# Performance work log

Measured on AMD Instinct MI355X. Metric: run time of the kernel, lower is better.

The kernel has to match this reference:

```python
import jax, jax.numpy as jnp
import numpy as np

EPS = 1e-5
ALPHA = 0.2  # leaky relu negative slope


def instance_norm(x):
    # x: [b, n, c]; torch InstanceNorm1d normalizes each (b, c) over the n dim (no affine)
    mean = jnp.mean(x, axis=1, keepdims=True)
    var = jnp.var(x, axis=1, keepdims=True)
    return (x - mean) * jax.lax.rsqrt(var + EPS)


def gat_layer(x, w, a_src, a_dst, bias):
    # x: [b, n, f_in], w: [h, f_in, f_out], a_src/a_dst: [h, f_out, 1], bias: [f_out]
    h_prime = jnp.einsum('bnf,hfo->bhno', x, w)              # [b, h, n, f_out]
    attn_src = jnp.einsum('bhno,hoi->bhni', h_prime, a_src)[..., 0]  # [b, h, n]
    attn_dst = jnp.einsum('bhno,hoi->bhni', h_prime, a_dst)[..., 0]  # [b, h, n]
    # outer-sum additive attention: attn[b,h,i,j] = src[b,h,i] + dst[b,h,j]
    attn = attn_src[:, :, :, None] + attn_dst[:, :, None, :]
    attn = jnp.where(attn >= 0, attn, ALPHA * attn)          # leaky relu
    attn = jax.nn.softmax(attn, axis=-1)
    out = jnp.einsum('bhnm,bhmo->bhno', attn, h_prime) + bias
    return out


def setup_inputs() -> dict:
    key = jax.random.key(0)
    ks = jax.random.split(key, 9)
    b, n = 16, 1024
    f0, f1, f2 = 32, 16, 32   # n_units
    h0, h1 = 4, 1             # n_heads

    def xavier(k, shape, gain=1.414):
        fan_in, fan_out = shape[-2], shape[-1]
        a = gain * np.sqrt(6.0 / (fan_in + fan_out))
        return jax.random.uniform(k, shape, jnp.float32, -a, a)

    return {
        'x': jax.random.normal(ks[0], (b, n, f0), jnp.float32),
        'w1': xavier(ks[1], (h0, f0, f1)),
        'a_src1': xavier(ks[2], (h0, f1, 1)),
        'a_dst1': xavier(ks[3], (h0, f1, 1)),
        'b1': jnp.zeros((f1,), jnp.float32),
        'w2': xavier(ks[4], (h1, f1 * h0, f2)),
        'a_src2': xavier(ks[5], (h1, f2, 1)),
        'a_dst2': xavier(ks[6], (h1, f2, 1)),
        'b2': jnp.zeros((f2,), jnp.float32),
    }


def reference(x, w1, a_src1, a_dst1, b1, w2, a_src2, a_dst2, b2):
    b, n = x.shape[:2]
    # layer 0
    x = instance_norm(x)
    out = gat_layer(x, w1, a_src1, a_dst1, b1)               # [b, h0, n, f1]
    x = jnp.transpose(out, (0, 2, 1, 3)).reshape(b, n, -1)   # [b, n, h0*f1]
    x = jax.nn.elu(x)
    # layer 1 (last): squeeze head dim
    x = instance_norm(x)
    out = gat_layer(x, w2, a_src2, a_dst2, b2)               # [b, 1, n, f2]
    return out[:, 0]                                          # [b, n, f2]
```

## Files before the change

### kernel.cpp

```cpp
#include <hip/hip_runtime.h>


namespace {
constexpr int Nn  = 1024;
constexpr int F0  = 32;
constexpr int F1n = 16;
constexpr int FH  = 64;
constexpr int F2n = 32;
constexpr float LOG2E = 1.4426950408889634f;
constexpr float EPS   = 1e-5f;
constexpr float ALPHA = 0.2f;
}

typedef __attribute__((ext_vector_type(8))) _Float16 half8;
typedef __attribute__((ext_vector_type(4))) float f32x4;

__global__ __launch_bounds__(256) void k_proj1(
    const float* __restrict__ x, const float* __restrict__ w1,
    const float* __restrict__ asrc, const float* __restrict__ adst,
    short* __restrict__ hpT_hi, short* __restrict__ hpT_lo,
    float* __restrict__ src, float* __restrict__ dst,
    float* __restrict__ statsAcc)
{
  const int b    = blockIdx.x >> 4;
  const int tile = blockIdx.x & 15;
  const int t    = threadIdx.x;
  const int r    = t & 63, h = t >> 6;

  __shared__ float  s_sum[8][33];
  __shared__ float  s_ssq[8][33];
  __shared__ float  s_mean[32], s_rstd[32];
  __shared__ float4 s_wt4[4 * F1n * (F0 / 4)];
  __shared__ float  s_as[64], s_ad[64];

  if (tile == 0 && t < 128) statsAcc[b * 128 + t] = 0.f;

  float* s_wt = reinterpret_cast<float*>(s_wt4);
  for (int idx = t; idx < 4 * F1n * F0; idx += 256) {
    const int f = idx & 31, ho = idx >> 5;
    s_wt[idx] = w1[((ho >> 4) * F0 + f) * F1n + (ho & 15)];
  }
  if (t < 64) { s_as[t] = asrc[t]; s_ad[t] = adst[t]; }

  const float* xb = x + (size_t)b * Nn * F0;
  {
    const int c = t & 31, seg = t >> 5;
    float sum = 0.f, ssq = 0.f;
#pragma unroll 8
    for (int nn = seg; nn < Nn; nn += 8) {
      float v = xb[nn * F0 + c];
      sum += v; ssq += v * v;
    }
    s_sum[seg][c] = sum; s_ssq[seg][c] = ssq;
  }
  __syncthreads();
  if (t < 32) {
    float s = 0.f, q = 0.f;
#pragma unroll
    for (int k = 0; k < 8; k++) { s += s_sum[k][t]; q += s_ssq[k][t]; }
    const float mean = s * (1.f / Nn);
    const float var  = fmaf(-mean, mean, q * (1.f / Nn));
    s_mean[t] = mean;
    s_rstd[t] = rsqrtf(var + EPS);
  }
  __syncthreads();

  const int n  = tile * 64 + r;
  const int bh = b * 4 + h;
  float4 xr[F0 / 4];
  const float4* xrow = reinterpret_cast<const float4*>(xb + (size_t)n * F0);
#pragma unroll
  for (int k = 0; k < F0 / 4; k++) {
    float4 v = xrow[k];
    v.x = (v.x - s_mean[k * 4 + 0]) * s_rstd[k * 4 + 0];
    v.y = (v.y - s_mean[k * 4 + 1]) * s_rstd[k * 4 + 1];
    v.z = (v.z - s_mean[k * 4 + 2]) * s_rstd[k * 4 + 2];
    v.w = (v.w - s_mean[k * 4 + 3]) * s_rstd[k * 4 + 3];
    xr[k] = v;
  }

  float sdot = 0.f, ddot = 0.f;
#pragma unroll 1
  for (int o = 0; o < F1n; o++) {
    float acc = 0.f;
#pragma unroll
    for (int k = 0; k < F0 / 4; k++) {
      const float4 wv = s_wt4[(h * F1n + o) * (F0 / 4) + k];
      const float4 xv = xr[k];
      acc = fmaf(xv.x, wv.x, acc); acc = fmaf(xv.y, wv.y, acc);
      acc = fmaf(xv.z, wv.z, acc); acc = fmaf(xv.w, wv.w, acc);
    }
    sdot = fmaf(acc, s_as[h * F1n + o], sdot);
    ddot = fmaf(acc, s_ad[h * F1n + o], ddot);
    const _Float16 hh = (_Float16)acc;
    const _Float16 hl = (_Float16)(acc - (float)hh);
    const size_t idx = ((size_t)bh * F1n + o) * Nn + n;
    hpT_hi[idx] = __builtin_bit_cast(short, hh);
    hpT_lo[idx] = __builtin_bit_cast(short, hl);
  }
  src[bh * Nn + n] = sdot;
  dst[bh * Nn + n] = ddot;
}

__global__ __launch_bounds__(256) void k_attn1(
    const short* __restrict__ hpT_hi, const short* __restrict__ hpT_lo,
    const float* __restrict__ src, const float* __restrict__ dst,
    const float* __restrict__ bias, float* __restrict__ x1,
    float* __restrict__ statsAcc)
{
  const int bh   = blockIdx.x >> 4;
  const int tile = blockIdx.x & 15;
  const int t    = threadIdx.x;
  const int w    = t >> 6;
  const int l    = t & 63;
  const int col  = l & 15;
  const int ks   = l >> 4;

  __shared__ float s_dst[Nn];
  __shared__ float s_red[4];
  __shared__ float s_ps[4][16];

  const float* dp = dst + bh * Nn;
  float lm = -1e30f;
  for (int j = t; j < Nn; j += 256) { float v = dp[j]; s_dst[j] = v; lm = fmaxf(lm, v); }
#pragma unroll
  for (int mask = 32; mask >= 1; mask >>= 1) lm = fmaxf(lm, __shfl_xor(lm, mask));
  if (l == 0) s_red[w] = lm;
  __syncthreads();
  const float dmax = fmaxf(fmaxf(s_red[0], s_red[1]), fmaxf(s_red[2], s_red[3]));

  const int i0 = tile * 64 + w * 16;
  const float si = src[bh * Nn + i0 + col];
  const float t0v = si + dmax;
  const float em  = fmaxf(t0v, ALPHA * t0v) * LOG2E;

  auto pexp = [&](float dv) {
    const float tt = si + dv;
    const float u  = fmaxf(tt, ALPHA * tt);
    return exp2f(fmaf(u, LOG2E, -em));
  };

  const half8* bph = reinterpret_cast<const half8*>(hpT_hi + (size_t)bh * F1n * Nn);
  const half8* bpl = reinterpret_cast<const half8*>(hpT_lo + (size_t)bh * F1n * Nn);
  f32x4 acc = {0.f, 0.f, 0.f, 0.f};
  float psum = 0.f;

#pragma unroll 2
  for (int jb = 0; jb < 32; ++jb) {
    const int jo = (jb << 5) | (ks << 3);
    const float4 dA = *reinterpret_cast<const float4*>(&s_dst[jo]);
    const float4 dB = *reinterpret_cast<const float4*>(&s_dst[jo + 4]);
    half8 af;
    const _Float16 q0 = (_Float16)pexp(dA.x); af[0] = q0;
    const _Float16 q1 = (_Float16)pexp(dA.y); af[1] = q1;
    const _Float16 q2 = (_Float16)pexp(dA.z); af[2] = q2;
    const _Float16 q3 = (_Float16)pexp(dA.w); af[3] = q3;
    const _Float16 q4 = (_Float16)pexp(dB.x); af[4] = q4;
    const _Float16 q5 = (_Float16)pexp(dB.y); af[5] = q5;
    const _Float16 q6 = (_Float16)pexp(dB.z); af[6] = q6;
    const _Float16 q7 = (_Float16)pexp(dB.w); af[7] = q7;
    psum += (((float)q0 + (float)q1) + ((float)q2 + (float)q3)) +
            (((float)q4 + (float)q5) + ((float)q6 + (float)q7));

    const half8 bh8 = bph[col * 128 + (jb << 2) + ks];
    const half8 bl8 = bpl[col * 128 + (jb << 2) + ks];
    acc = __builtin_amdgcn_mfma_f32_16x16x32_f16(af, bh8, acc, 0, 0, 0);
    acc = __builtin_amdgcn_mfma_f32_16x16x32_f16(af, bl8, acc, 0, 0, 0);
  }

  psum += __shfl_xor(psum, 16);
  psum += __shfl_xor(psum, 32);
  if (l < 16) s_ps[w][col] = psum;
  __syncthreads();

  const int b = bh >> 2, h = bh & 3;
  const float bc = bias[col];
  float sv = 0.f, sq = 0.f;
#pragma unroll
  for (int r = 0; r < 4; ++r) {
    const int row = ks * 4 + r;
    const float inv = 1.f / s_ps[w][row];
    float v = fmaf(acc[r], inv, bc);
    v = v > 0.f ? v : exp2f(v * LOG2E) - 1.f;
    x1[((size_t)(b * Nn + i0 + row)) * FH + h * F1n + col] = v;
    sv += v; sq += v * v;
  }
  sv += __shfl_xor(sv, 16); sq += __shfl_xor(sq, 16);
  sv += __shfl_xor(sv, 32); sq += __shfl_xor(sq, 32);
  if (l < 16) {
    const int ch = h * F1n + col;
    atomicAdd(&statsAcc[b * 128 + ch], sv);
    atomicAdd(&statsAcc[b * 128 + 64 + ch], sq);
  }
}

__global__ __launch_bounds__(256) void k_proj2(
    const float* __restrict__ x1, const float* __restrict__ statsAcc,
    const float* __restrict__ w2,
    const float* __restrict__ asrc, const float* __restrict__ adst,
    short* __restrict__ hpT_hi, short* __restrict__ hpT_lo,
    float* __restrict__ src, float* __restrict__ dst)
{
  const int b    = blockIdx.x >> 4;
  const int tile = blockIdx.x & 15;
  const int t    = threadIdx.x;
  const int r    = t & 63, og = t >> 6;

  __shared__ float  s_mean[64], s_rstd[64];
  __shared__ float4 s_wt4[F2n * (FH / 4)];
  __shared__ float  s_as[F2n], s_ad[F2n];
  __shared__ float  s_sd[4][64][2];

  float* s_wt = reinterpret_cast<float*>(s_wt4);
  for (int idx = t; idx < F2n * FH; idx += 256) {
    const int f = idx & 63, o = idx >> 6;
    s_wt[idx] = w2[f * F2n + o];
  }
  if (t < F2n) { s_as[t] = asrc[t]; s_ad[t] = adst[t]; }
  if (t < 64) {
    const float s = statsAcc[b * 128 + t];
    const float q = statsAcc[b * 128 + 64 + t];
    const float mean = s * (1.f / Nn);
    const float var  = fmaf(-mean, mean, q * (1.f / Nn));
    s_mean[t] = mean;
    s_rstd[t] = rsqrtf(var + EPS);
  }
  __syncthreads();

  const int n    = tile * 64 + r;
  const int base = b * Nn + n;
  float4 xr[FH / 4];
  const float4* xrow = reinterpret_cast<const float4*>(
      x1 + (size_t)b * Nn * FH + (size_t)n * FH);
#pragma unroll
  for (int k = 0; k < FH / 4; k++) {
    float4 v = xrow[k];
    v.x = (v.x - s_mean[k * 4 + 0]) * s_rstd[k * 4 + 0];
    v.y = (v.y - s_mean[k * 4 + 1]) * s_rstd[k * 4 + 1];
    v.z = (v.z - s_mean[k * 4 + 2]) * s_rstd[k * 4 + 2];
    v.w = (v.w - s_mean[k * 4 + 3]) * s_rstd[k * 4 + 3];
    xr[k] = v;
  }

  float sdot = 0.f, ddot = 0.f;
#pragma unroll 1
  for (int oo = 0; oo < 8; oo++) {
    const int o = og * 8 + oo;
    float acc = 0.f;
#pragma unroll
    for (int k = 0; k < FH / 4; k++) {
      const float4 wv = s_wt4[o * (FH / 4) + k];
      const float4 xv = xr[k];
      acc = fmaf(xv.x, wv.x, acc); acc = fmaf(xv.y, wv.y, acc);
      acc = fmaf(xv.z, wv.z, acc); acc = fmaf(xv.w, wv.w, acc);
    }
    sdot = fmaf(acc, s_as[o], sdot);
    ddot = fmaf(acc, s_ad[o], ddot);
    const _Float16 hh = (_Float16)acc;
    const _Float16 hl = (_Float16)(acc - (float)hh);
    const size_t idx = ((size_t)b * F2n + o) * Nn + n;
    hpT_hi[idx] = __builtin_bit_cast(short, hh);
    hpT_lo[idx] = __builtin_bit_cast(short, hl);
  }

  s_sd[og][r][0] = sdot; s_sd[og][r][1] = ddot;
  __syncthreads();
  if (og == 0) {
    float s = 0.f, d = 0.f;
#pragma unroll
    for (int g = 0; g < 4; g++) { s += s_sd[g][r][0]; d += s_sd[g][r][1]; }
    src[base] = s;
    dst[base] = d;
  }
}

__global__ __launch_bounds__(256) void k_attn2(
    const short* __restrict__ hpT_hi, const short* __restrict__ hpT_lo,
    const float* __restrict__ src, const float* __restrict__ dst,
    const float* __restrict__ bias, float* __restrict__ out)
{
  const int b    = blockIdx.x >> 6;
  const int tile = blockIdx.x & 63;
  const int t    = threadIdx.x;
  const int jq   = t >> 6;
  const int l    = t & 63;
  const int col  = l & 15;
  const int ks   = l >> 4;

  __shared__ float s_dst[Nn];
  __shared__ float s_red[4];
  __shared__ float s_comb[3][64][9];
  __shared__ float s_ps[16];

  const float* dp = dst + b * Nn;
  float lm = -1e30f;
  for (int j = t; j < Nn; j += 256) { float v = dp[j]; s_dst[j] = v; lm = fmaxf(lm, v); }
#pragma unroll
  for (int mask = 32; mask >= 1; mask >>= 1) lm = fmaxf(lm, __shfl_xor(lm, mask));
  if (l == 0) s_red[jq] = lm;
  __syncthreads();
  const float dmax = fmaxf(fmaxf(s_red[0], s_red[1]), fmaxf(s_red[2], s_red[3]));

  const int i0 = tile * 16;
  const float si = src[b * Nn + i0 + col];
  const float t0v = si + dmax;
  const float em  = fmaxf(t0v, ALPHA * t0v) * LOG2E;

  auto pexp = [&](float dv) {
    const float tt = si + dv;
    const float u  = fmaxf(tt, ALPHA * tt);
    return exp2f(fmaf(u, LOG2E, -em));
  };

  const half8* bph = reinterpret_cast<const half8*>(hpT_hi + (size_t)b * F2n * Nn);
  const half8* bpl = reinterpret_cast<const half8*>(hpT_lo + (size_t)b * F2n * Nn);
  f32x4 acc0 = {0.f, 0.f, 0.f, 0.f};
  f32x4 acc1 = {0.f, 0.f, 0.f, 0.f};
  float psum = 0.f;

#pragma unroll 2
  for (int kb = 0; kb < 8; ++kb) {
    const int jb = jq * 8 + kb;
    const int jo = (jb << 5) | (ks << 3);
    const float4 dA = *reinterpret_cast<const float4*>(&s_dst[jo]);
    const float4 dB = *reinterpret_cast<const float4*>(&s_dst[jo + 4]);
    half8 af;
    const _Float16 q0 = (_Float16)pexp(dA.x); af[0] = q0;
    const _Float16 q1 = (_Float16)pexp(dA.y); af[1] = q1;
    const _Float16 q2 = (_Float16)pexp(dA.z); af[2] = q2;
    const _Float16 q3 = (_Float16)pexp(dA.w); af[3] = q3;
    const _Float16 q4 = (_Float16)pexp(dB.x); af[4] = q4;
    const _Float16 q5 = (_Float16)pexp(dB.y); af[5] = q5;
    const _Float16 q6 = (_Float16)pexp(dB.z); af[6] = q6;
    const _Float16 q7 = (_Float16)pexp(dB.w); af[7] = q7;
    psum += (((float)q0 + (float)q1) + ((float)q2 + (float)q3)) +
            (((float)q4 + (float)q5) + ((float)q6 + (float)q7));

    const half8 bh0 = bph[col * 128 + (jb << 2) + ks];
    const half8 bl0 = bpl[col * 128 + (jb << 2) + ks];
    const half8 bh1 = bph[(col + 16) * 128 + (jb << 2) + ks];
    const half8 bl1 = bpl[(col + 16) * 128 + (jb << 2) + ks];
    acc0 = __builtin_amdgcn_mfma_f32_16x16x32_f16(af, bh0, acc0, 0, 0, 0);
    acc0 = __builtin_amdgcn_mfma_f32_16x16x32_f16(af, bl0, acc0, 0, 0, 0);
    acc1 = __builtin_amdgcn_mfma_f32_16x16x32_f16(af, bh1, acc1, 0, 0, 0);
    acc1 = __builtin_amdgcn_mfma_f32_16x16x32_f16(af, bl1, acc1, 0, 0, 0);
  }

  if (jq > 0) {
#pragma unroll
    for (int r = 0; r < 4; ++r) {
      s_comb[jq - 1][l][r]     = acc0[r];
      s_comb[jq - 1][l][r + 4] = acc1[r];
    }
    s_comb[jq - 1][l][8] = psum;
  }
  __syncthreads();

  if (jq == 0) {
#pragma unroll
    for (int g = 0; g < 3; ++g) {
#pragma unroll
      for (int r = 0; r < 4; ++r) {
        acc0[r] += s_comb[g][l][r];
        acc1[r] += s_comb[g][l][r + 4];
      }
      psum += s_comb[g][l][8];
    }
    psum += __shfl_xor(psum, 16);
    psum += __shfl_xor(psum, 32);
    if (l < 16) s_ps[col] = psum;

    const float bc0 = bias[col];
    const float bc1 = bias[col + 16];
#pragma unroll
    for (int r = 0; r < 4; ++r) {
      const int row = ks * 4 + r;
      const float inv = 1.f / s_ps[row];
      float* op = out + ((size_t)(b * Nn + i0 + row)) * F2n;
      op[col]      = fmaf(acc0[r], inv, bc0);
      op[col + 16] = fmaf(acc1[r], inv, bc1);
    }
  }
}

extern "C" void kernel_launch(void* const* d_in, const int* in_sizes, int n_in,
                              void* d_out, int out_size, void* d_ws, size_t ws_size,
                              hipStream_t stream) {
  (void)in_sizes; (void)n_in; (void)out_size; (void)ws_size;
  const float* x   = (const float*)d_in[0];
  const float* w1  = (const float*)d_in[1];
  const float* as1 = (const float*)d_in[2];
  const float* ad1 = (const float*)d_in[3];
  const float* b1  = (const float*)d_in[4];
  const float* w2  = (const float*)d_in[5];
  const float* as2 = (const float*)d_in[6];
  const float* ad2 = (const float*)d_in[7];
  const float* b2  = (const float*)d_in[8];
  float* out = (float*)d_out;

  float* ws = (float*)d_ws;
  short* hpT1_hi = (short*)ws;
  short* hpT1_lo = (short*)(ws + 524288);
  short* hpT2_hi = (short*)(ws + 1048576);
  short* hpT2_lo = (short*)(ws + 1048576 + 262144);
  float* x1      = ws + 1048576 + 524288;
  float* src1    = x1 + 1048576;
  float* dst1    = src1 + 65536;
  float* src2    = dst1 + 65536;
  float* dst2    = src2 + 16384;
  float* statsA  = dst2 + 16384;

  k_proj1<<<256, 256, 0, stream>>>(x, w1, as1, ad1, hpT1_hi, hpT1_lo, src1, dst1, statsA);
  k_attn1<<<1024, 256, 0, stream>>>(hpT1_hi, hpT1_lo, src1, dst1, b1, x1, statsA);
  k_proj2<<<256, 256, 0, stream>>>(x1, statsA, w2, as2, ad2, hpT2_hi, hpT2_lo, src2, dst2);
  k_attn2<<<1024, 256, 0, stream>>>(hpT2_hi, hpT2_lo, src2, dst2, b2, out);
}
```

Before: 142.3 us.

## Fuse four stage kernels into one persistent kernel with grid barriers

Merges the projection and attention stages of both layers into a single 1024-block kernel. The stages are separated by atomic-counter grid barriers, and a shared-memory union lets every stage reuse the same LDS. The aim is to remove three kernel launch boundaries and the drain/ramp gaps between them. In exchange it needs all 1024 blocks co-resident (4 per CU), which is checked via an occupancy query with a fallback to the original four launches. It also adds a memset and a host occupancy call on every launch, and spin-wait barriers that idle the 768 blocks doing nothing during the projection stages.

```diff
diff --git a/kernel.cpp b/kernel.cpp
--- a/kernel.cpp
+++ b/kernel.cpp
@@ -15,32 +15,44 @@
 typedef __attribute__((ext_vector_type(8))) _Float16 half8;
 typedef __attribute__((ext_vector_type(4))) float f32x4;
 
-__global__ __launch_bounds__(256) void k_proj1(
+union alignas(16) Smem {
+  struct { float sum[8][33], ssq[8][33], mean[32], rstd[32], wt[2048], as[64], ad[64]; } p1;
+  struct { float dst[Nn], red[4], ps[4][16]; } p2;
+  struct { float mean[64], rstd[64], wt[2048], as[32], ad[32], sd[4][64][2]; } p3;
+  struct { float dst[Nn], red[4], comb[3][64][9], ps[16]; } p4;
+};
+
+__device__ __forceinline__ void grid_barrier(unsigned* c, unsigned nblk) {
+  __syncthreads();
+  if (threadIdx.x == 0) {
+    __threadfence();
+    __hip_atomic_fetch_add(c, 1u, __ATOMIC_RELAXED, __HIP_MEMORY_SCOPE_AGENT);
+    while (__hip_atomic_load(c, __ATOMIC_RELAXED, __HIP_MEMORY_SCOPE_AGENT) < nblk)
+      __builtin_amdgcn_s_sleep(2);
+    __threadfence();
+  }
+  __syncthreads();
+}
+
+__device__ __forceinline__ void proj1_body(
+    int bid, int t, Smem& sm,
     const float* __restrict__ x, const float* __restrict__ w1,
     const float* __restrict__ asrc, const float* __restrict__ adst,
     short* __restrict__ hpT_hi, short* __restrict__ hpT_lo,
     float* __restrict__ src, float* __restrict__ dst,
     float* __restrict__ statsAcc)
 {
-  const int b    = blockIdx.x >> 4;
-  const int tile = blockIdx.x & 15;
-  const int t    = threadIdx.x;
+  const int b    = bid >> 4;
+  const int tile = bid & 15;
   const int r    = t & 63, h = t >> 6;
 
-  __shared__ float  s_sum[8][33];
-  __shared__ float  s_ssq[8][33];
-  __shared__ float  s_mean[32], s_rstd[32];
-  __shared__ float4 s_wt4[4 * F1n * (F0 / 4)];
-  __shared__ float  s_as[64], s_ad[64];
-
   if (tile == 0 && t < 128) statsAcc[b * 128 + t] = 0.f;
 
-  float* s_wt = reinterpret_cast<float*>(s_wt4);
   for (int idx = t; idx < 4 * F1n * F0; idx += 256) {
     const int f = idx & 31, ho = idx >> 5;
-    s_wt[idx] = w1[((ho >> 4) * F0 + f) * F1n + (ho & 15)];
-  }
-  if (t < 64) { s_as[t] = asrc[t]; s_ad[t] = adst[t]; }
+    sm.p1.wt[idx] = w1[((ho >> 4) * F0 + f) * F1n + (ho & 15)];
+  }
+  if (t < 64) { sm.p1.as[t] = asrc[t]; sm.p1.ad[t] = adst[t]; }
 
   const float* xb = x + (size_t)b * Nn * F0;
   {
@@ -51,17 +63,17 @@
       float v = xb[nn * F0 + c];
       sum += v; ssq += v * v;
     }
-    s_sum[seg][c] = sum; s_ssq[seg][c] = ssq;
+    sm.p1.sum[seg][c] = sum; sm.p1.ssq[seg][c] = ssq;
   }
   __syncthreads();
   if (t < 32) {
     float s = 0.f, q = 0.f;
 #pragma unroll
-    for (int k = 0; k < 8; k++) { s += s_sum[k][t]; q += s_ssq[k][t]; }
+    for (int k = 0; k < 8; k++) { s += sm.p1.sum[k][t]; q += sm.p1.ssq[k][t]; }
     const float mean = s * (1.f / Nn);
     const float var  = fmaf(-mean, mean, q * (1.f / Nn));
-    s_mean[t] = mean;
-    s_rstd[t] = rsqrtf(var + EPS);
+    sm.p1.mean[t] = mean;
+    sm.p1.rstd[t] = rsqrtf(var + EPS);
   }
   __syncthreads();
 
@@ -72,26 +84,27 @@
 #pragma unroll
   for (int k = 0; k < F0 / 4; k++) {
     float4 v = xrow[k];
-    v.x = (v.x - s_mean[k * 4 + 0]) * s_rstd[k * 4 + 0];
-    v.y = (v.y - s_mean[k * 4 + 1]) * s_rstd[k * 4 + 1];
-    v.z = (v.z - s_mean[k * 4 + 2]) * s_rstd[k * 4 + 2];
-    v.w = (v.w - s_mean[k * 4 + 3]) * s_rstd[k * 4 + 3];
+    v.x = (v.x - sm.p1.mean[k * 4 + 0]) * sm.p1.rstd[k * 4 + 0];
+    v.y = (v.y - sm.p1.mean[k * 4 + 1]) * sm.p1.rstd[k * 4 + 1];
+    v.z = (v.z - sm.p1.mean[k * 4 + 2]) * sm.p1.rstd[k * 4 + 2];
+    v.w = (v.w - sm.p1.mean[k * 4 + 3]) * sm.p1.rstd[k * 4 + 3];
     xr[k] = v;
   }
 
+  const float4* wt4 = reinterpret_cast<const float4*>(sm.p1.wt);
   float sdot = 0.f, ddot = 0.f;
 #pragma unroll 1
   for (int o = 0; o < F1n; o++) {
     float acc = 0.f;
 #pragma unroll
     for (int k = 0; k < F0 / 4; k++) {
-      const float4 wv = s_wt4[(h * F1n + o) * (F0 / 4) + k];
+      const float4 wv = wt4[(h * F1n + o) * (F0 / 4) + k];
       const float4 xv = xr[k];
       acc = fmaf(xv.x, wv.x, acc); acc = fmaf(xv.y, wv.y, acc);
       acc = fmaf(xv.z, wv.z, acc); acc = fmaf(xv.w, wv.w, acc);
     }
-    sdot = fmaf(acc, s_as[h * F1n + o], sdot);
-    ddot = fmaf(acc, s_ad[h * F1n + o], ddot);
+    sdot = fmaf(acc, sm.p1.as[h * F1n + o], sdot);
+    ddot = fmaf(acc, sm.p1.ad[h * F1n + o], ddot);
     const _Float16 hh = (_Float16)acc;
     const _Float16 hl = (_Float16)(acc - (float)hh);
     const size_t idx = ((size_t)bh * F1n + o) * Nn + n;
@@ -102,32 +115,29 @@
   dst[bh * Nn + n] = ddot;
 }
 
-__global__ __launch_bounds__(256) void k_attn1(
+__device__ __forceinline__ void attn1_body(
+    int bid, int t, Smem& sm,
     const short* __restrict__ hpT_hi, const short* __restrict__ hpT_lo,
     const float* __restrict__ src, const float* __restrict__ dst,
     const float* __restrict__ bias, float* __restrict__ x1,
     float* __restrict__ statsAcc)
 {
-  const int bh   = blockIdx.x >> 4;
-  const int tile = blockIdx.x & 15;
-  const int t    = threadIdx.x;
+  const int bh   = bid >> 4;
+  const int tile = bid & 15;
   const int w    = t >> 6;
   const int l    = t & 63;
   const int col  = l & 15;
   const int ks   = l >> 4;
 
-  __shared__ float s_dst[Nn];
-  __shared__ float s_red[4];
-  __shared__ float s_ps[4][16];
-
   const float* dp = dst + bh * Nn;
   float lm = -1e30f;
-  for (int j = t; j < Nn; j += 256) { float v = dp[j]; s_dst[j] = v; lm = fmaxf(lm, v); }
+  for (int j = t; j < Nn; j += 256) { float v = dp[j]; sm.p2.dst[j] = v; lm = fmaxf(lm, v); }
 #pragma unroll
   for (int mask = 32; mask >= 1; mask >>= 1) lm = fmaxf(lm, __shfl_xor(lm, mask));
-  if (l == 0) s_red[w] = lm;
-  __syncthreads();
-  const float dmax = fmaxf(fmaxf(s_red[0], s_red[1]), fmaxf(s_red[2], s_red[3]));
+  if (l == 0) sm.p2.red[w] = lm;
+  __syncthreads();
+  const float dmax = fmaxf(fmaxf(sm.p2.red[0], sm.p2.red[1]),
+                           fmaxf(sm.p2.red[2], sm.p2.red[3]));
 
   const int i0 = tile * 64 + w * 16;
   const float si = src[bh * Nn + i0 + col];
@@ -148,8 +158,8 @@
 #pragma unroll 2
   for (int jb = 0; jb < 32; ++jb) {
     const int jo = (jb << 5) | (ks << 3);
-    const float4 dA = *reinterpret_cast<const float4*>(&s_dst[jo]);
-    const float4 dB = *reinterpret_cast<const float4*>(&s_dst[jo + 4]);
+    const float4 dA = *reinterpret_cast<const float4*>(&sm.p2.dst[jo]);
+    const float4 dB = *reinterpret_cast<const float4*>(&sm.p2.dst[jo + 4]);
     half8 af;
     const _Float16 q0 = (_Float16)pexp(dA.x); af[0] = q0;
     const _Float16 q1 = (_Float16)pexp(dA.y); af[1] = q1;
@@ -170,7 +180,7 @@
 
   psum += __shfl_xor(psum, 16);
   psum += __shfl_xor(psum, 32);
-  if (l < 16) s_ps[w][col] = psum;
+  if (l < 16) sm.p2.ps[w][col] = psum;
   __syncthreads();
 
   const int b = bh >> 2, h = bh & 3;
@@ -179,7 +189,7 @@
 #pragma unroll
   for (int r = 0; r < 4; ++r) {
     const int row = ks * 4 + r;
-    const float inv = 1.f / s_ps[w][row];
+    const float inv = 1.f / sm.p2.ps[w][row];
     float v = fmaf(acc[r], inv, bc);
     v = v > 0.f ? v : exp2f(v * LOG2E) - 1.f;
     x1[((size_t)(b * Nn + i0 + row)) * FH + h * F1n + col] = v;
@@ -194,36 +204,30 @@
   }
 }
 
-__global__ __launch_bounds__(256) void k_proj2(
+__device__ __forceinline__ void proj2_body(
+    int bid, int t, Smem& sm,
     const float* __restrict__ x1, const float* __restrict__ statsAcc,
     const float* __restrict__ w2,
     const float* __restrict__ asrc, const float* __restrict__ adst,
     short* __restrict__ hpT_hi, short* __restrict__ hpT_lo,
     float* __restrict__ src, float* __restrict__ dst)
 {
-  const int b    = blockIdx.x >> 4;
-  const int tile = blockIdx.x & 15;
-  const int t    = threadIdx.x;
+  const int b    = bid >> 4;
+  const int tile = bid & 15;
   const int r    = t & 63, og = t >> 6;
 
-  __shared__ float  s_mean[64], s_rstd[64];
-  __shared__ float4 s_wt4[F2n * (FH / 4)];
-  __shared__ float  s_as[F2n], s_ad[F2n];
-  __shared__ float  s_sd[4][64][2];
-
-  float* s_wt = reinterpret_cast<float*>(s_wt4);
   for (int idx = t; idx < F2n * FH; idx += 256) {
     const int f = idx & 63, o = idx >> 6;
-    s_wt[idx] = w2[f * F2n + o];
-  }
-  if (t < F2n) { s_as[t] = asrc[t]; s_ad[t] = adst[t]; }
+    sm.p3.wt[idx] = w2[f * F2n + o];
+  }
+  if (t < F2n) { sm.p3.as[t] = asrc[t]; sm.p3.ad[t] = adst[t]; }
   if (t < 64) {
     const float s = statsAcc[b * 128 + t];
     const float q = statsAcc[b * 128 + 64 + t];
     const float mean = s * (1.f / Nn);
     const float var  = fmaf(-mean, mean, q * (1.f / Nn));
-    s_mean[t] = mean;
-    s_rstd[t] = rsqrtf(var + EPS);
+    sm.p3.mean[t] = mean;
+    sm.p3.rstd[t] = rsqrtf(var + EPS);
   }
   __syncthreads();
 
@@ -235,13 +239,14 @@
 #pragma unroll
   for (int k = 0; k < FH / 4; k++) {
     float4 v = xrow[k];
-    v.x = (v.x - s_mean[k * 4 + 0]) * s_rstd[k * 4 + 0];
-    v.y = (v.y - s_mean[k * 4 + 1]) * s_rstd[k * 4 + 1];
-    v.z = (v.z - s_mean[k * 4 + 2]) * s_rstd[k * 4 + 2];
-    v.w = (v.w - s_mean[k * 4 + 3]) * s_rstd[k * 4 + 3];
+    v.x = (v.x - sm.p3.mean[k * 4 + 0]) * sm.p3.rstd[k * 4 + 0];
+    v.y = (v.y - sm.p3.mean[k * 4 + 1]) * sm.p3.rstd[k * 4 + 1];
+    v.z = (v.z - sm.p3.mean[k * 4 + 2]) * sm.p3.rstd[k * 4 + 2];
+    v.w = (v.w - sm.p3.mean[k * 4 + 3]) * sm.p3.rstd[k * 4 + 3];
     xr[k] = v;
   }
 
+  const float4* wt4 = reinterpret_cast<const float4*>(sm.p3.wt);
   float sdot = 0.f, ddot = 0.f;
 #pragma unroll 1
   for (int oo = 0; oo < 8; oo++) {
@@ -249,13 +254,13 @@
     float acc = 0.f;
 #pragma unroll
     for (int k = 0; k < FH / 4; k++) {
-      const float4 wv = s_wt4[o * (FH / 4) + k];
+      const float4 wv = wt4[o * (FH / 4) + k];
       const float4 xv = xr[k];
       acc = fmaf(xv.x, wv.x, acc); acc = fmaf(xv.y, wv.y, acc);
       acc = fmaf(xv.z, wv.z, acc); acc = fmaf(xv.w, wv.w, acc);
     }
-    sdot = fmaf(acc, s_as[o], sdot);
-    ddot = fmaf(acc, s_ad[o], ddot);
+    sdot = fmaf(acc, sm.p3.as[o], sdot);
+    ddot = fmaf(acc, sm.p3.ad[o], ddot);
     const _Float16 hh = (_Float16)acc;
     const _Float16 hl = (_Float16)(acc - (float)hh);
     const size_t idx = ((size_t)b * F2n + o) * Nn + n;
@@ -263,43 +268,39 @@
     hpT_lo[idx] = __builtin_bit_cast(short, hl);
   }
 
-  s_sd[og][r][0] = sdot; s_sd[og][r][1] = ddot;
+  sm.p3.sd[og][r][0] = sdot; sm.p3.sd[og][r][1] = ddot;
   __syncthreads();
   if (og == 0) {
     float s = 0.f, d = 0.f;
 #pragma unroll
-    for (int g = 0; g < 4; g++) { s += s_sd[g][r][0]; d += s_sd[g][r][1]; }
+    for (int g = 0; g < 4; g++) { s += sm.p3.sd[g][r][0]; d += sm.p3.sd[g][r][1]; }
     src[base] = s;
     dst[base] = d;
   }
 }
 
-__global__ __launch_bounds__(256) void k_attn2(
+__device__ __forceinline__ void attn2_body(
+    int bid, int t, Smem& sm,
     const short* __restrict__ hpT_hi, const short* __restrict__ hpT_lo,
     const float* __restrict__ src, const float* __restrict__ dst,
     const float* __restrict__ bias, float* __restrict__ out)
 {
-  const int b    = blockIdx.x >> 6;
-  const int tile = blockIdx.x & 63;
-  const int t    = threadIdx.x;
+  const int b    = bid >> 6;
+  const int tile = bid & 63;
   const int jq   = t >> 6;
   const int l    = t & 63;
   const int col  = l & 15;
   const int ks   = l >> 4;
 
-  __shared__ float s_dst[Nn];
-  __shared__ float s_red[4];
-  __shared__ float s_comb[3][64][9];
-  __shared__ float s_ps[16];
-
   const float* dp = dst + b * Nn;
   float lm = -1e30f;
-  for (int j = t; j < Nn; j += 256) { float v = dp[j]; s_dst[j] = v; lm = fmaxf(lm, v); }
+  for (int j = t; j < Nn; j += 256) { float v = dp[j]; sm.p4.dst[j] = v; lm = fmaxf(lm, v); }
 #pragma unroll
   for (int mask = 32; mask >= 1; mask >>= 1) lm = fmaxf(lm, __shfl_xor(lm, mask));
-  if (l == 0) s_red[jq] = lm;
-  __syncthreads();
-  const float dmax = fmaxf(fmaxf(s_red[0], s_red[1]), fmaxf(s_red[2], s_red[3]));
+  if (l == 0) sm.p4.red[jq] = lm;
+  __syncthreads();
+  const float dmax = fmaxf(fmaxf(sm.p4.red[0], sm.p4.red[1]),
+                           fmaxf(sm.p4.red[2], sm.p4.red[3]));
 
   const int i0 = tile * 16;
   const float si = src[b * Nn + i0 + col];
@@ -322,8 +323,8 @@
   for (int kb = 0; kb < 8; ++kb) {
     const int jb = jq * 8 + kb;
     const int jo = (jb << 5) | (ks << 3);
-    const float4 dA = *reinterpret_cast<const float4*>(&s_dst[jo]);
-    const float4 dB = *reinterpret_cast<const float4*>(&s_dst[jo + 4]);
+    const float4 dA = *reinterpret_cast<const float4*>(&sm.p4.dst[jo]);
+    const float4 dB = *reinterpret_cast<const float4*>(&sm.p4.dst[jo + 4]);
     half8 af;
     const _Float16 q0 = (_Float16)pexp(dA.x); af[0] = q0;
     const _Float16 q1 = (_Float16)pexp(dA.y); af[1] = q1;
@@ -349,10 +350,10 @@
   if (jq > 0) {
 #pragma unroll
     for (int r = 0; r < 4; ++r) {
-      s_comb[jq - 1][l][r]     = acc0[r];
-      s_comb[jq - 1][l][r + 4] = acc1[r];
-    }
-    s_comb[jq - 1][l][8] = psum;
+      sm.p4.comb[jq - 1][l][r]     = acc0[r];
+      sm.p4.comb[jq - 1][l][r + 4] = acc1[r];
+    }
+    sm.p4.comb[jq - 1][l][8] = psum;
   }
   __syncthreads();
 
@@ -361,27 +362,75 @@
     for (int g = 0; g < 3; ++g) {
 #pragma unroll
       for (int r = 0; r < 4; ++r) {
-        acc0[r] += s_comb[g][l][r];
-        acc1[r] += s_comb[g][l][r + 4];
+        acc0[r] += sm.p4.comb[g][l][r];
+        acc1[r] += sm.p4.comb[g][l][r + 4];
       }
-      psum += s_comb[g][l][8];
+      psum += sm.p4.comb[g][l][8];
     }
     psum += __shfl_xor(psum, 16);
     psum += __shfl_xor(psum, 32);
-    if (l < 16) s_ps[col] = psum;
+    if (l < 16) sm.p4.ps[col] = psum;
 
     const float bc0 = bias[col];
     const float bc1 = bias[col + 16];
 #pragma unroll
     for (int r = 0; r < 4; ++r) {
       const int row = ks * 4 + r;
-      const float inv = 1.f / s_ps[row];
+      const float inv = 1.f / sm.p4.ps[row];
       float* op = out + ((size_t)(b * Nn + i0 + row)) * F2n;
       op[col]      = fmaf(acc0[r], inv, bc0);
       op[col + 16] = fmaf(acc1[r], inv, bc1);
     }
   }
 }
+
+__global__ __launch_bounds__(256, 4) void k_fused(
+    const float* __restrict__ x, const float* __restrict__ w1,
+    const float* __restrict__ as1, const float* __restrict__ ad1,
+    const float* __restrict__ b1,  const float* __restrict__ w2,
+    const float* __restrict__ as2, const float* __restrict__ ad2,
+    const float* __restrict__ b2,
+    short* hpT1_hi, short* hpT1_lo, short* hpT2_hi, short* hpT2_lo,
+    float* x1, float* src1, float* dst1, float* src2, float* dst2,
+    float* statsA, float* out, unsigned* bars)
+{
+  __shared__ Smem sm;
+  const int bid = blockIdx.x, t = threadIdx.x;
+
+  if (bid < 256)
+    proj1_body(bid, t, sm, x, w1, as1, ad1, hpT1_hi, hpT1_lo, src1, dst1, statsA);
+  grid_barrier(bars + 0, 1024u);
+
+  attn1_body(bid, t, sm, hpT1_hi, hpT1_lo, src1, dst1, b1, x1, statsA);
+  grid_barrier(bars + 1, 1024u);
+
+  if (bid < 256)
+    proj2_body(bid, t, sm, x1, statsA, w2, as2, ad2, hpT2_hi, hpT2_lo, src2, dst2);
+  grid_barrier(bars + 2, 1024u);
+
+  attn2_body(bid, t, sm, hpT2_hi, hpT2_lo, src2, dst2, b2, out);
+}
+
+__global__ __launch_bounds__(256) void k_proj1(
+    const float* x, const float* w1, const float* as1, const float* ad1,
+    short* hpT_hi, short* hpT_lo, float* src, float* dst, float* statsA)
+{ __shared__ Smem sm; proj1_body(blockIdx.x, threadIdx.x, sm, x, w1, as1, ad1, hpT_hi, hpT_lo, src, dst, statsA); }
+
+__global__ __launch_bounds__(256) void k_attn1(
+    const short* hpT_hi, const short* hpT_lo, const float* src, const float* dst,
+    const float* bias, float* x1, float* statsA)
+{ __shared__ Smem sm; attn1_body(blockIdx.x, threadIdx.x, sm, hpT_hi, hpT_lo, src, dst, bias, x1, statsA); }
+
+__global__ __launch_bounds__(256) void k_proj2(
+    const float* x1, const float* statsA, const float* w2,
+    const float* as2, const float* ad2,
+    short* hpT_hi, short* hpT_lo, float* src, float* dst)
+{ __shared__ Smem sm; proj2_body(blockIdx.x, threadIdx.x, sm, x1, statsA, w2, as2, ad2, hpT_hi, hpT_lo, src, dst); }
+
+__global__ __launch_bounds__(256) void k_attn2(
+    const short* hpT_hi, const short* hpT_lo, const float* src, const float* dst,
+    const float* bias, float* out)
+{ __shared__ Smem sm; attn2_body(blockIdx.x, threadIdx.x, sm, hpT_hi, hpT_lo, src, dst, bias, out); }
 
 extern "C" void kernel_launch(void* const* d_in, const int* in_sizes, int n_in,
                               void* d_out, int out_size, void* d_ws, size_t ws_size,
@@ -409,9 +458,20 @@
   float* src2    = dst1 + 65536;
   float* dst2    = src2 + 16384;
   float* statsA  = dst2 + 16384;
-
-  k_proj1<<<256, 256, 0, stream>>>(x, w1, as1, ad1, hpT1_hi, hpT1_lo, src1, dst1, statsA);
-  k_attn1<<<1024, 256, 0, stream>>>(hpT1_hi, hpT1_lo, src1, dst1, b1, x1, statsA);
-  k_proj2<<<256, 256, 0, stream>>>(x1, statsA, w2, as2, ad2, hpT2_hi, hpT2_lo, src2, dst2);
-  k_attn2<<<1024, 256, 0, stream>>>(hpT2_hi, hpT2_lo, src2, dst2, b2, out);
-}
+  unsigned* bars = (unsigned*)(statsA + 2048);
+
+  (void)hipMemsetAsync(bars, 0, 3 * sizeof(unsigned), stream);
+
+  int maxB = 0;
+  hipError_t e = hipOccupancyMaxActiveBlocksPerMultiprocessor(&maxB, k_fused, 256, 0);
+  if (e == hipSuccess && maxB >= 4) {
+    k_fused<<<1024, 256, 0, stream>>>(x, w1, as1, ad1, b1, w2, as2, ad2, b2,
+                                      hpT1_hi, hpT1_lo, hpT2_hi, hpT2_lo,
+                                      x1, src1, dst1, src2, dst2, statsA, out, bars);
+  } else {
+    k_proj1<<<256, 256, 0, stream>>>(x, w1, as1, ad1, hpT1_hi, hpT1_lo, src1, dst1, statsA);
+    k_attn1<<<1024, 256, 0, stream>>>(hpT1_hi, hpT1_lo, src1, dst1, b1, x1, statsA);
+    k_proj2<<<256, 256, 0, stream>>>(x1, statsA, w2, as2, ad2, hpT2_hi, hpT2_lo, src2, dst2);
+    k_attn2<<<1024, 256, 0, stream>>>(hpT2_hi, hpT2_lo, src2, dst2, b2, out);
+  }
+}
```

New measurement: 146.0 us. +2.6%, slower.
